# Kernel tuning notes

Measured on AMD Instinct MI355X. Metric: run time of the kernel, lower is better.

Reference implementation:

```python
import jax, jax.numpy as jnp
import numpy as np


def segment_softmax(logits, seg, num_seg):
    m = jax.ops.segment_max(logits, seg, num_segments=num_seg)
    z = jnp.exp(logits - m[seg])
    s = jax.ops.segment_sum(z, seg, num_segments=num_seg)
    return z / s[seg]


def hconv(x_lin, edge_node, edge_he, num_nodes, num_edges, bias, alpha=None):
    # PyG HypergraphConv (heads=1, concat=True): D^-1 H W_e B^-1 H^T X Theta
    ones = jnp.ones(edge_node.shape[0], x_lin.dtype)
    D = jax.ops.segment_sum(ones, edge_node, num_segments=num_nodes)
    Dinv = jnp.where(D > 0, 1.0 / D, 0.0)
    Bd = jax.ops.segment_sum(ones, edge_he, num_segments=num_edges)
    Binv = jnp.where(Bd > 0, 1.0 / Bd, 0.0)
    # node -> hyperedge
    msg = Binv[edge_he][:, None] * x_lin[edge_node]
    if alpha is not None:
        msg = alpha[:, None] * msg
    e = jax.ops.segment_sum(msg, edge_he, num_segments=num_edges)
    # hyperedge -> node
    msg2 = Dinv[edge_node][:, None] * e[edge_he]
    if alpha is not None:
        msg2 = alpha[:, None] * msg2
    out = jax.ops.segment_sum(msg2, edge_node, num_segments=num_nodes)
    return out + bias


def reference(c_it, medicine_it, c_embeddings, m_embeddings, W_conv, b_conv, W_gat, att, b_gat, he_attr):
    nd = c_embeddings.shape[0]  # all indicators are 1 -> nonzero indexing is identity
    nm = m_embeddings.shape[0]
    oc = W_conv.shape[0]

    # diagnosis hypergraph: single hyperedge containing all diseases
    dia_x = c_embeddings @ W_conv.T  # [nd, oc]
    dia_nf = hconv(dia_x, jnp.arange(nd), jnp.zeros(nd, jnp.int32), nd, 1, b_conv)

    # medicine hypergraph: single hyperedge containing all medicines
    med_x = m_embeddings @ W_conv.T  # [nm, oc]
    med_nf = hconv(med_x, jnp.arange(nm), jnp.zeros(nm, jnp.int32), nm, 1, b_conv)

    # dia-med hypergraph: nd hyperedges, hyperedge d = {disease d} U {all medicines}
    comb = jnp.concatenate([c_embeddings, m_embeddings], axis=0)  # [nd+nm, in]
    x_lin = comb @ W_gat.T                                        # [nd+nm, oc]
    he_lin = he_attr @ W_gat.T                                    # [nd, oc]
    med_nodes = jnp.arange(nd, nd + nm)
    edge_node = jnp.concatenate(
        [jnp.arange(nd)[:, None], jnp.broadcast_to(med_nodes[None, :], (nd, nm))], axis=1
    ).reshape(-1)                              # [nd*(nm+1)]
    edge_he = jnp.repeat(jnp.arange(nd), nm + 1)

    # attention (attention_mode='node'): alpha from source node + hyperedge attr, softmax per hyperedge
    a_node = x_lin @ att[:oc]   # [nd+nm]
    a_he = he_lin @ att[oc:]    # [nd]
    logits = jax.nn.leaky_relu(a_node[edge_node] + a_he[edge_he], 0.2)
    alpha = segment_softmax(logits, edge_he, nd)

    dm_nf = hconv(x_lin, edge_node, edge_he, nd + nm, nd, b_gat, alpha)  # [nd+nm, oc]

    disease_final = jnp.concatenate([dm_nf[:nd], dia_nf], axis=1)   # [nd, 2*oc]
    medicine_final = jnp.concatenate([dm_nf[nd:], med_nf], axis=1)  # [nm, 2*oc]
    return jnp.concatenate([disease_final, medicine_final], axis=0)  # [nd+nm, 2*oc]


def setup_inputs() -> dict:
    key = jax.random.key(0)
    ks = jax.random.split(key, 8)
    ND, NM, IN, OUT = 2048, 512, 256, 128
    s = 0.05
    return {
        "c_it": jnp.ones((ND,), jnp.int32),
        "medicine_it": jnp.ones((NM,), jnp.int32),
        "c_embeddings": jax.random.normal(ks[0], (ND, IN), jnp.float32),
        "m_embeddings": jax.random.normal(ks[1], (NM, IN), jnp.float32),
        "W_conv": jax.random.normal(ks[2], (OUT, IN), jnp.float32) * s,
        "b_conv": jax.random.normal(ks[3], (OUT,), jnp.float32) * s,
        "W_gat": jax.random.normal(ks[4], (OUT, IN), jnp.float32) * s,
        "att": jax.random.normal(ks[5], (2 * OUT,), jnp.float32) * s,
        "b_gat": jax.random.normal(ks[6], (OUT,), jnp.float32) * s,
        "he_attr": jax.random.normal(ks[7], (ND, IN), jnp.float32),
    }
```

## Files before the change

kernel.cpp:

```cpp
#include <hip/hip_runtime.h>

#define ND 2048
#define NM 512
#define DIN 256
#define OC 128
#define NTOT 2560
#define NE 513

#define WS_PARTC 0
#define WS_PARTM (WS_PARTC + 512*256)
#define WS_AHE   (WS_PARTM + 128*256)
#define WS_ANODE (WS_AHE + ND)
#define WS_CD    (WS_ANODE + NTOT)
#define WS_XLIN  (WS_CD + ND)
#define WS_DIA   (WS_XLIN + NTOT*OC)
#define WS_MED   (WS_DIA + OC)

__device__ __forceinline__ float lrelu(float x) { return x > 0.f ? x : 0.2f * x; }

__global__ void __launch_bounds__(256) K1(
        const float* __restrict__ c_emb, const float* __restrict__ m_emb,
        const float* __restrict__ W_gat, const float* __restrict__ att,
        const float* __restrict__ he_attr, float* __restrict__ ws) {
    const int b = blockIdx.x, t = threadIdx.x;
    if (b < 640) {
        __shared__ float row[4][DIN];
        __shared__ float sA[4][OC];
        const int d0 = b * 4;
#pragma unroll
        for (int p = 0; p < 2; ++p) {
            const int idx = p * 256 + t;
            const int r = idx >> 7, c = idx & 127;
            const int d = d0 + r;
            const float* src = (d < ND) ? c_emb + (size_t)d * DIN
                                        : m_emb + (size_t)(d - ND) * DIN;
            const float2 u = ((const float2*)src)[c];
            row[r][2 * c]     = u.x;
            row[r][2 * c + 1] = u.y;
        }
        __syncthreads();
        {
            const float pc = row[0][t] + row[1][t] + row[2][t] + row[3][t];
            if (b < 512) ws[WS_PARTC + b * 256 + t] = pc;
            else         ws[WS_PARTM + (b - 512) * 256 + t] = pc;
        }
        const int o = t & (OC - 1), h = t >> 7;
        float a0 = 0.f, a1 = 0.f;
        const float4* wr = (const float4*)(W_gat + (size_t)o * DIN);
        const float* r0 = row[2 * h];
        const float* r1 = row[2 * h + 1];
#pragma unroll 8
        for (int v = 0; v < 64; ++v) {
            const float4 w = wr[v];
            const int ib = 4 * v;
            a0 = fmaf(r0[ib],     w.x, a0);
            a0 = fmaf(r0[ib + 1], w.y, a0);
            a0 = fmaf(r0[ib + 2], w.z, a0);
            a0 = fmaf(r0[ib + 3], w.w, a0);
            a1 = fmaf(r1[ib],     w.x, a1);
            a1 = fmaf(r1[ib + 1], w.y, a1);
            a1 = fmaf(r1[ib + 2], w.z, a1);
            a1 = fmaf(r1[ib + 3], w.w, a1);
        }
        ws[WS_XLIN + (size_t)(d0 + 2 * h) * OC + o]     = a0;
        ws[WS_XLIN + (size_t)(d0 + 2 * h + 1) * OC + o] = a1;
        const float at = att[o];
        sA[2 * h][o]     = a0 * at;
        sA[2 * h + 1][o] = a1 * at;
        __syncthreads();
#pragma unroll
        for (int st = 64; st >= 1; st >>= 1) {
            if (t < 4 * st) {
                const int r = t / st, i = t - r * st;
                sA[r][i] += sA[r][i + st];
            }
            __syncthreads();
        }
        if (t < 4) ws[WS_ANODE + d0 + t] = sA[t][0];
    } else {
        __shared__ float satt[OC];
        __shared__ float we[DIN];
        const int q = b - 640;
        if (t < OC) satt[t] = att[OC + t];
        __syncthreads();
        float acc = 0.f;
#pragma unroll 8
        for (int o = 0; o < OC; ++o)
            acc = fmaf(W_gat[(size_t)o * DIN + t], satt[o], acc);
        we[t] = acc;
        __syncthreads();
        const int r = t >> 5, l = t & 31;
        const int d = q * 8 + r;
        const float* he = he_attr + (size_t)d * DIN;
        float ah = 0.f;
#pragma unroll
        for (int i = l; i < DIN; i += 32) ah = fmaf(he[i], we[i], ah);
#pragma unroll
        for (int m = 1; m < 32; m <<= 1) ah += __shfl_xor(ah, m, 32);
        if (l == 0) ws[WS_AHE + d] = ah;
    }
}

__global__ void __launch_bounds__(256) K2(
        const float* __restrict__ W_conv, const float* __restrict__ b_conv,
        const float* __restrict__ b_gat, float* __restrict__ ws,
        float* __restrict__ out) {
    const int b = blockIdx.x, t = threadIdx.x;
    if (b == 256) {
        __shared__ float mc[DIN], mm[DIN];
        float sc = 0.f, sm = 0.f;
        for (int bb = 0; bb < 512; ++bb) sc += ws[WS_PARTC + bb * 256 + t];
        for (int bb = 0; bb < 128; ++bb) sm += ws[WS_PARTM + bb * 256 + t];
        mc[t] = sc * (1.f / ND);
        mm[t] = sm * (1.f / NM);
        __syncthreads();
        if (t < OC) {
            const float4* wr = (const float4*)(W_conv + (size_t)t * DIN);
            float a = 0.f, m2 = 0.f;
#pragma unroll 8
            for (int v = 0; v < 64; ++v) {
                const float4 w = wr[v];
                const int ib = 4 * v;
                a  = fmaf(mc[ib], w.x, a);     a  = fmaf(mc[ib + 1], w.y, a);
                a  = fmaf(mc[ib + 2], w.z, a); a  = fmaf(mc[ib + 3], w.w, a);
                m2 = fmaf(mm[ib], w.x, m2);    m2 = fmaf(mm[ib + 1], w.y, m2);
                m2 = fmaf(mm[ib + 2], w.z, m2); m2 = fmaf(mm[ib + 3], w.w, m2);
            }
            const float bc = b_conv[t];
            ws[WS_DIA + t] = a + bc;
            ws[WS_MED + t] = m2 + bc;
        }
        return;
    }
    __shared__ float zbuf[NE][8];
    __shared__ float anm[NM];
    __shared__ float ec[8][OC];
    anm[t]       = ws[WS_ANODE + ND + t];
    anm[t + 256] = ws[WS_ANODE + ND + 256 + t];
    __syncthreads();
    {
        const int r = t >> 5, l = t & 31;
        const int d = b * 8 + r;
        const float ah = ws[WS_AHE + d];
        const float an_d = ws[WS_ANODE + d];
        float lmax = -3.4e38f;
        for (int j = l; j < NE; j += 32) {
            const float v = (j == 0) ? an_d : anm[j - 1];
            const float lg = lrelu(v + ah);
            zbuf[j][r] = lg;
            lmax = fmaxf(lmax, lg);
        }
#pragma unroll
        for (int m = 1; m < 32; m <<= 1) lmax = fmaxf(lmax, __shfl_xor(lmax, m, 32));
        float ss = 0.f;
        for (int j = l; j < NE; j += 32) {
            const float z = __expf(zbuf[j][r] - lmax);
            zbuf[j][r] = z;
            ss += z;
        }
#pragma unroll
        for (int m = 1; m < 32; m <<= 1) ss += __shfl_xor(ss, m, 32);
        const float inv = 1.f / ss;
        if (l == 0) ws[WS_CD + d] = lmax + __logf(ss);
        for (int j = l; j < NE; j += 32) zbuf[j][r] *= inv;
    }
    __syncthreads();
    const int o = t & (OC - 1), h = t >> 7;
    float acc[8] = {0, 0, 0, 0, 0, 0, 0, 0};
    const float* xm = ws + WS_XLIN + (size_t)ND * OC;
    for (int j = h * 256; j < h * 256 + 256; ++j) {
        const float xv = xm[(size_t)j * OC + o];
        const float4* zr = (const float4*)zbuf[j + 1];
        const float4 za = zr[0], zb4 = zr[1];
        acc[0] = fmaf(za.x,  xv, acc[0]);
        acc[1] = fmaf(za.y,  xv, acc[1]);
        acc[2] = fmaf(za.z,  xv, acc[2]);
        acc[3] = fmaf(za.w,  xv, acc[3]);
        acc[4] = fmaf(zb4.x, xv, acc[4]);
        acc[5] = fmaf(zb4.y, xv, acc[5]);
        acc[6] = fmaf(zb4.z, xv, acc[6]);
        acc[7] = fmaf(zb4.w, xv, acc[7]);
    }
    if (h == 1) {
#pragma unroll
        for (int k = 0; k < 8; ++k) ec[k][o] = acc[k];
    }
    __syncthreads();
    if (h == 0) {
        const float bg = b_gat[o];
#pragma unroll
        for (int k = 0; k < 8; ++k) {
            const int dd = b * 8 + k;
            const float a0 = zbuf[0][k];
            const float xown = ws[WS_XLIN + (size_t)dd * OC + o];
            const float ev = fmaf(a0, xown, acc[k] + ec[k][o]) * (1.f / NE);
            ws[WS_XLIN + (size_t)dd * OC + o] = ev;
            out[(size_t)dd * 2 * OC + o] = fmaf(a0, ev, bg);
        }
    }
}

__global__ void __launch_bounds__(256) K3(
        const float* __restrict__ b_gat, const float* __restrict__ ws,
        float* __restrict__ out) {
    const int b = blockIdx.x, t = threadIdx.x;
    const int o = t & (OC - 1), h = t >> 7;
    if (b < 256) {
        __shared__ float zb[ND][2];
        __shared__ float ec2[2][OC];
        const int m0 = b * 2;
        const float an0 = ws[WS_ANODE + ND + m0];
        const float an1 = ws[WS_ANODE + ND + m0 + 1];
        for (int dd = t; dd < ND; dd += 256) {
            const float ahv = ws[WS_AHE + dd];
            const float cdv = ws[WS_CD + dd];
            zb[dd][0] = __expf(lrelu(an0 + ahv) - cdv);
            zb[dd][1] = __expf(lrelu(an1 + ahv) - cdv);
        }
        __syncthreads();
        float a0 = 0.f, a1 = 0.f;
        const float* e = ws + WS_XLIN;
        for (int dd = h * 1024; dd < h * 1024 + 1024; ++dd) {
            const float ev = e[(size_t)dd * OC + o];
            a0 = fmaf(zb[dd][0], ev, a0);
            a1 = fmaf(zb[dd][1], ev, a1);
        }
        if (h == 1) { ec2[0][o] = a0; ec2[1][o] = a1; }
        __syncthreads();
        if (h == 0) {
            const float bg = b_gat[o];
            const float mv = ws[WS_MED + o];
            out[(size_t)(ND + m0) * 2 * OC + o]          = fmaf(a0 + ec2[0][o], 1.f / ND, bg);
            out[(size_t)(ND + m0) * 2 * OC + OC + o]     = mv;
            out[(size_t)(ND + m0 + 1) * 2 * OC + o]      = fmaf(a1 + ec2[1][o], 1.f / ND, bg);
            out[(size_t)(ND + m0 + 1) * 2 * OC + OC + o] = mv;
        }
    } else {
        const int q = b - 256;
        const float dv = ws[WS_DIA + o];
#pragma unroll
        for (int rr = 0; rr < 16; ++rr) {
            const int d = q * 32 + 2 * rr + h;
            out[(size_t)d * 2 * OC + OC + o] = dv;
        }
    }
}

extern "C" void kernel_launch(void* const* d_in, const int* in_sizes, int n_in,
                              void* d_out, int out_size, void* d_ws, size_t ws_size,
                              hipStream_t stream) {
    const float* c_emb   = (const float*)d_in[2];
    const float* m_emb   = (const float*)d_in[3];
    const float* W_conv  = (const float*)d_in[4];
    const float* b_conv  = (const float*)d_in[5];
    const float* W_gat   = (const float*)d_in[6];
    const float* att     = (const float*)d_in[7];
    const float* b_gat   = (const float*)d_in[8];
    const float* he_attr = (const float*)d_in[9];
    float* ws  = (float*)d_ws;
    float* out = (float*)d_out;

    hipLaunchKernelGGL(K1, dim3(896), dim3(256), 0, stream,
                       c_emb, m_emb, W_gat, att, he_attr, ws);
    hipLaunchKernelGGL(K2, dim3(257), dim3(256), 0, stream,
                       W_conv, b_conv, b_gat, ws, out);
    hipLaunchKernelGGL(K3, dim3(320), dim3(256), 0, stream, b_gat, ws, out);
}
```

Before: 151.4 us.

## Increase per-block row tiling in K1 and medicine tiling in K3

```diff
diff --git a/kernel.cpp b/kernel.cpp
--- a/kernel.cpp
+++ b/kernel.cpp
@@ -8,8 +8,8 @@
 #define NE 513
 
 #define WS_PARTC 0
-#define WS_PARTM (WS_PARTC + 512*256)
-#define WS_AHE   (WS_PARTM + 128*256)
+#define WS_PARTM (WS_PARTC + 256*256)
+#define WS_AHE   (WS_PARTM + 64*256)
 #define WS_ANODE (WS_AHE + ND)
 #define WS_CD    (WS_ANODE + NTOT)
 #define WS_XLIN  (WS_CD + ND)
@@ -23,12 +23,12 @@
         const float* __restrict__ W_gat, const float* __restrict__ att,
         const float* __restrict__ he_attr, float* __restrict__ ws) {
     const int b = blockIdx.x, t = threadIdx.x;
-    if (b < 640) {
-        __shared__ float row[4][DIN];
-        __shared__ float sA[4][OC];
-        const int d0 = b * 4;
-#pragma unroll
-        for (int p = 0; p < 2; ++p) {
+    if (b < 320) {
+        __shared__ float row[8][DIN];
+        __shared__ float sA[8][OC];
+        const int d0 = b * 8;
+#pragma unroll
+        for (int p = 0; p < 4; ++p) {
             const int idx = p * 256 + t;
             const int r = idx >> 7, c = idx & 127;
             const int d = d0 + r;
@@ -40,47 +40,53 @@
         }
         __syncthreads();
         {
-            const float pc = row[0][t] + row[1][t] + row[2][t] + row[3][t];
-            if (b < 512) ws[WS_PARTC + b * 256 + t] = pc;
-            else         ws[WS_PARTM + (b - 512) * 256 + t] = pc;
+            float pc = 0.f;
+#pragma unroll
+            for (int r = 0; r < 8; ++r) pc += row[r][t];
+            if (b < 256) ws[WS_PARTC + b * 256 + t] = pc;
+            else         ws[WS_PARTM + (b - 256) * 256 + t] = pc;
         }
         const int o = t & (OC - 1), h = t >> 7;
-        float a0 = 0.f, a1 = 0.f;
-        const float4* wr = (const float4*)(W_gat + (size_t)o * DIN);
-        const float* r0 = row[2 * h];
-        const float* r1 = row[2 * h + 1];
-#pragma unroll 8
+        float a0 = 0.f, a1 = 0.f, a2 = 0.f, a3 = 0.f;
+        const float4* wr  = (const float4*)(W_gat + (size_t)o * DIN);
+        const float4* r0v = (const float4*)(row[4 * h]);
+        const float4* r1v = (const float4*)(row[4 * h + 1]);
+        const float4* r2v = (const float4*)(row[4 * h + 2]);
+        const float4* r3v = (const float4*)(row[4 * h + 3]);
+#pragma unroll 4
         for (int v = 0; v < 64; ++v) {
-            const float4 w = wr[v];
-            const int ib = 4 * v;
-            a0 = fmaf(r0[ib],     w.x, a0);
-            a0 = fmaf(r0[ib + 1], w.y, a0);
-            a0 = fmaf(r0[ib + 2], w.z, a0);
-            a0 = fmaf(r0[ib + 3], w.w, a0);
-            a1 = fmaf(r1[ib],     w.x, a1);
-            a1 = fmaf(r1[ib + 1], w.y, a1);
-            a1 = fmaf(r1[ib + 2], w.z, a1);
-            a1 = fmaf(r1[ib + 3], w.w, a1);
-        }
-        ws[WS_XLIN + (size_t)(d0 + 2 * h) * OC + o]     = a0;
-        ws[WS_XLIN + (size_t)(d0 + 2 * h + 1) * OC + o] = a1;
+            const float4 w  = wr[v];
+            const float4 x0 = r0v[v], x1 = r1v[v], x2 = r2v[v], x3 = r3v[v];
+            a0 = fmaf(x0.x, w.x, a0); a0 = fmaf(x0.y, w.y, a0);
+            a0 = fmaf(x0.z, w.z, a0); a0 = fmaf(x0.w, w.w, a0);
+            a1 = fmaf(x1.x, w.x, a1); a1 = fmaf(x1.y, w.y, a1);
+            a1 = fmaf(x1.z, w.z, a1); a1 = fmaf(x1.w, w.w, a1);
+            a2 = fmaf(x2.x, w.x, a2); a2 = fmaf(x2.y, w.y, a2);
+            a2 = fmaf(x2.z, w.z, a2); a2 = fmaf(x2.w, w.w, a2);
+            a3 = fmaf(x3.x, w.x, a3); a3 = fmaf(x3.y, w.y, a3);
+            a3 = fmaf(x3.z, w.z, a3); a3 = fmaf(x3.w, w.w, a3);
+        }
+        float* xl = ws + WS_XLIN + (size_t)(d0 + 4 * h) * OC + o;
+        xl[0 * OC] = a0; xl[1 * OC] = a1; xl[2 * OC] = a2; xl[3 * OC] = a3;
         const float at = att[o];
-        sA[2 * h][o]     = a0 * at;
-        sA[2 * h + 1][o] = a1 * at;
+        sA[4 * h][o]     = a0 * at;
+        sA[4 * h + 1][o] = a1 * at;
+        sA[4 * h + 2][o] = a2 * at;
+        sA[4 * h + 3][o] = a3 * at;
         __syncthreads();
 #pragma unroll
         for (int st = 64; st >= 1; st >>= 1) {
-            if (t < 4 * st) {
-                const int r = t / st, i = t - r * st;
+            for (int idx = t; idx < 8 * st; idx += 256) {
+                const int r = idx / st, i = idx - r * st;
                 sA[r][i] += sA[r][i + st];
             }
             __syncthreads();
         }
-        if (t < 4) ws[WS_ANODE + d0 + t] = sA[t][0];
+        if (t < 8) ws[WS_ANODE + d0 + t] = sA[t][0];
     } else {
         __shared__ float satt[OC];
         __shared__ float we[DIN];
-        const int q = b - 640;
+        const int q = b - 320;
         if (t < OC) satt[t] = att[OC + t];
         __syncthreads();
         float acc = 0.f;
@@ -90,14 +96,17 @@
         we[t] = acc;
         __syncthreads();
         const int r = t >> 5, l = t & 31;
-        const int d = q * 8 + r;
-        const float* he = he_attr + (size_t)d * DIN;
-        float ah = 0.f;
-#pragma unroll
-        for (int i = l; i < DIN; i += 32) ah = fmaf(he[i], we[i], ah);
-#pragma unroll
-        for (int m = 1; m < 32; m <<= 1) ah += __shfl_xor(ah, m, 32);
-        if (l == 0) ws[WS_AHE + d] = ah;
+#pragma unroll
+        for (int k = 0; k < 4; ++k) {
+            const int d = q * 32 + k * 8 + r;
+            const float* he = he_attr + (size_t)d * DIN;
+            float ah = 0.f;
+#pragma unroll
+            for (int i = l; i < DIN; i += 32) ah = fmaf(he[i], we[i], ah);
+#pragma unroll
+            for (int m = 1; m < 32; m <<= 1) ah += __shfl_xor(ah, m, 32);
+            if (l == 0) ws[WS_AHE + d] = ah;
+        }
     }
 }
 
@@ -109,8 +118,8 @@
     if (b == 256) {
         __shared__ float mc[DIN], mm[DIN];
         float sc = 0.f, sm = 0.f;
-        for (int bb = 0; bb < 512; ++bb) sc += ws[WS_PARTC + bb * 256 + t];
-        for (int bb = 0; bb < 128; ++bb) sm += ws[WS_PARTM + bb * 256 + t];
+        for (int bb = 0; bb < 256; ++bb) sc += ws[WS_PARTC + bb * 256 + t];
+        for (int bb = 0; bb < 64;  ++bb) sm += ws[WS_PARTM + bb * 256 + t];
         mc[t] = sc * (1.f / ND);
         mm[t] = sm * (1.f / NM);
         __syncthreads();
@@ -121,9 +130,9 @@
             for (int v = 0; v < 64; ++v) {
                 const float4 w = wr[v];
                 const int ib = 4 * v;
-                a  = fmaf(mc[ib], w.x, a);     a  = fmaf(mc[ib + 1], w.y, a);
-                a  = fmaf(mc[ib + 2], w.z, a); a  = fmaf(mc[ib + 3], w.w, a);
-                m2 = fmaf(mm[ib], w.x, m2);    m2 = fmaf(mm[ib + 1], w.y, m2);
+                a  = fmaf(mc[ib], w.x, a);      a  = fmaf(mc[ib + 1], w.y, a);
+                a  = fmaf(mc[ib + 2], w.z, a);  a  = fmaf(mc[ib + 3], w.w, a);
+                m2 = fmaf(mm[ib], w.x, m2);     m2 = fmaf(mm[ib + 1], w.y, m2);
                 m2 = fmaf(mm[ib + 2], w.z, m2); m2 = fmaf(mm[ib + 3], w.w, m2);
             }
             const float bc = b_conv[t];
@@ -205,38 +214,54 @@
         float* __restrict__ out) {
     const int b = blockIdx.x, t = threadIdx.x;
     const int o = t & (OC - 1), h = t >> 7;
-    if (b < 256) {
-        __shared__ float zb[ND][2];
-        __shared__ float ec2[2][OC];
-        const int m0 = b * 2;
-        const float an0 = ws[WS_ANODE + ND + m0];
-        const float an1 = ws[WS_ANODE + ND + m0 + 1];
-        for (int dd = t; dd < ND; dd += 256) {
-            const float ahv = ws[WS_AHE + dd];
-            const float cdv = ws[WS_CD + dd];
-            zb[dd][0] = __expf(lrelu(an0 + ahv) - cdv);
-            zb[dd][1] = __expf(lrelu(an1 + ahv) - cdv);
-        }
-        __syncthreads();
-        float a0 = 0.f, a1 = 0.f;
+    if (b < 64) {
+        __shared__ float zb[256][8];
+        __shared__ float ec2[8][OC];
+        __shared__ float anm8[8];
+        const int m0 = b * 8;
+        if (t < 8) anm8[t] = ws[WS_ANODE + ND + m0 + t];
+        __syncthreads();
+        float acc[8] = {0, 0, 0, 0, 0, 0, 0, 0};
         const float* e = ws + WS_XLIN;
-        for (int dd = h * 1024; dd < h * 1024 + 1024; ++dd) {
-            const float ev = e[(size_t)dd * OC + o];
-            a0 = fmaf(zb[dd][0], ev, a0);
-            a1 = fmaf(zb[dd][1], ev, a1);
-        }
-        if (h == 1) { ec2[0][o] = a0; ec2[1][o] = a1; }
+        for (int c = 0; c < 8; ++c) {
+            for (int idx = t; idx < 2048; idx += 256) {
+                const int dd = idx >> 3, mi = idx & 7;
+                const int d = c * 256 + dd;
+                zb[dd][mi] = __expf(lrelu(anm8[mi] + ws[WS_AHE + d]) - ws[WS_CD + d]);
+            }
+            __syncthreads();
+            for (int dd = h * 128; dd < h * 128 + 128; ++dd) {
+                const float ev = e[(size_t)(c * 256 + dd) * OC + o];
+                const float4* zr = (const float4*)zb[dd];
+                const float4 za = zr[0], zb4 = zr[1];
+                acc[0] = fmaf(za.x,  ev, acc[0]);
+                acc[1] = fmaf(za.y,  ev, acc[1]);
+                acc[2] = fmaf(za.z,  ev, acc[2]);
+                acc[3] = fmaf(za.w,  ev, acc[3]);
+                acc[4] = fmaf(zb4.x, ev, acc[4]);
+                acc[5] = fmaf(zb4.y, ev, acc[5]);
+                acc[6] = fmaf(zb4.z, ev, acc[6]);
+                acc[7] = fmaf(zb4.w, ev, acc[7]);
+            }
+            __syncthreads();
+        }
+        if (h == 1) {
+#pragma unroll
+            for (int k = 0; k < 8; ++k) ec2[k][o] = acc[k];
+        }
         __syncthreads();
         if (h == 0) {
             const float bg = b_gat[o];
             const float mv = ws[WS_MED + o];
-            out[(size_t)(ND + m0) * 2 * OC + o]          = fmaf(a0 + ec2[0][o], 1.f / ND, bg);
-            out[(size_t)(ND + m0) * 2 * OC + OC + o]     = mv;
-            out[(size_t)(ND + m0 + 1) * 2 * OC + o]      = fmaf(a1 + ec2[1][o], 1.f / ND, bg);
-            out[(size_t)(ND + m0 + 1) * 2 * OC + OC + o] = mv;
+#pragma unroll
+            for (int k = 0; k < 8; ++k) {
+                const int m = m0 + k;
+                out[(size_t)(ND + m) * 2 * OC + o]      = fmaf(acc[k] + ec2[k][o], 1.f / ND, bg);
+                out[(size_t)(ND + m) * 2 * OC + OC + o] = mv;
+            }
         }
     } else {
-        const int q = b - 256;
+        const int q = b - 64;
         const float dv = ws[WS_DIA + o];
 #pragma unroll
         for (int rr = 0; rr < 16; ++rr) {
@@ -260,9 +285,9 @@
     float* ws  = (float*)d_ws;
     float* out = (float*)d_out;
 
-    hipLaunchKernelGGL(K1, dim3(896), dim3(256), 0, stream,
+    hipLaunchKernelGGL(K1, dim3(384), dim3(256), 0, stream,
                        c_emb, m_emb, W_gat, att, he_attr, ws);
     hipLaunchKernelGGL(K2, dim3(257), dim3(256), 0, stream,
                        W_conv, b_conv, b_gat, ws, out);
-    hipLaunchKernelGGL(K3, dim3(320), dim3(256), 0, stream, b_gat, ws, out);
-}
+    hipLaunchKernelGGL(K3, dim3(128), dim3(256), 0, stream, b_gat, ws, out);
+}
```

New measurement: 351.7 us. 132% more time.
